# Kernel optimization log

Measured on AMD Instinct MI355X. Metric: run time of the kernel, lower is better.

The kernel has to match this reference:

```python
import jax, jax.numpy as jnp
import numpy as np
import math

D_MODEL = 1024
NUM_HEADS = 16
B, L = 2, 2048
# scale_level=0, patch_time_span=1 -> effective_stride=1
PERIODS = (1.0, 30.0)
WEIGHTS = (0.8, 0.4)
SIGMAS = (0.5, 2.0)


def setup_inputs() -> dict:
    key = jax.random.key(0)
    ks = jax.random.split(key, 10)
    s = 1.0 / math.sqrt(D_MODEL)
    inp = {
        "x": jax.random.normal(ks[0], (B, L, D_MODEL), dtype=jnp.float32),
        "Wq": jax.random.normal(ks[1], (D_MODEL, D_MODEL), dtype=jnp.float32) * s,
        "bq": jax.random.normal(ks[2], (D_MODEL,), dtype=jnp.float32) * 0.01,
        "Wk": jax.random.normal(ks[3], (D_MODEL, D_MODEL), dtype=jnp.float32) * s,
        "bk": jax.random.normal(ks[4], (D_MODEL,), dtype=jnp.float32) * 0.01,
        "Wv": jax.random.normal(ks[5], (D_MODEL, D_MODEL), dtype=jnp.float32) * s,
        "bv": jax.random.normal(ks[6], (D_MODEL,), dtype=jnp.float32) * 0.01,
        "Wo": jax.random.normal(ks[7], (D_MODEL, D_MODEL), dtype=jnp.float32) * s,
        "bo": jax.random.normal(ks[8], (D_MODEL,), dtype=jnp.float32) * 0.01,
        "prior_lambda": jnp.asarray(2.0, dtype=jnp.float32),
    }
    return inp


def _gaussian_mask(length):
    idx = jnp.arange(length, dtype=jnp.float32)
    delta = jnp.abs(idx[:, None] - idx[None, :])  # [L, L]
    mask = jnp.zeros_like(delta)
    for p, w, sigma in zip(PERIODS, WEIGHTS, SIGMAS):
        if p < 0.2:
            continue
        mask = mask + w * jnp.exp(-((delta - p) ** 2) / (2.0 * sigma ** 2))
    return mask


def reference(x, Wq, bq, Wk, bk, Wv, bv, Wo, bo, prior_lambda):
    Bx, Lx, D = x.shape
    H = NUM_HEADS
    hd = D // H

    def split_heads(t):  # [B, L, D] -> [B, H, L, hd]
        return t.reshape(Bx, Lx, H, hd).transpose(0, 2, 1, 3)

    Q = split_heads(x @ Wq.T + bq)
    K = split_heads(x @ Wk.T + bk)
    V = split_heads(x @ Wv.T + bv)

    scores = jnp.einsum("bhqd,bhkd->bhqk", Q, K) / math.sqrt(hd)
    scores = scores + prior_lambda * _gaussian_mask(Lx)[None, None, :, :]
    attn = jax.nn.softmax(scores, axis=-1)
    out = jnp.einsum("bhqk,bhkd->bhqd", attn, V)
    out = out.transpose(0, 2, 1, 3).reshape(Bx, Lx, D)
    return out @ Wo.T + bo
```

## Files before the change

### kernel.cpp

```cpp
#include <hip/hip_runtime.h>

#define D_MODEL 1024
#define SEQ_L   2048
#define NHEADS  16
#define HDIM    64
#define NROWS   4096

#define QSCALE 0.18033688011112042f
#define LOG2E  1.4426950408889634f

#if __has_builtin(__builtin_amdgcn_exp2f)
#define EXP2F(x) __builtin_amdgcn_exp2f(x)
#else
#define EXP2F(x) __expf((x) * 0.6931471805599453f)
#endif

typedef __attribute__((ext_vector_type(8))) short short8;
typedef __attribute__((ext_vector_type(4))) short short4v;
typedef __attribute__((ext_vector_type(4))) float floatx4;
typedef __attribute__((ext_vector_type(4))) unsigned short ushort4v;
typedef unsigned short ushort;

static __device__ __forceinline__ ushort f2bf(float f) {
    unsigned int u = __float_as_uint(f);
    u += 0x7FFFu + ((u >> 16) & 1u);
    return (ushort)(u >> 16);
}

static __device__ __forceinline__ floatx4 mfma16(short8 a, short8 b, floatx4 c) {
    return __builtin_amdgcn_mfma_f32_16x16x32_bf16(a, b, c, 0, 0, 0);
}

static __device__ __forceinline__ floatx4 mfma16k16(short4v a, short4v b, floatx4 c) {
    return __builtin_amdgcn_mfma_f32_16x16x16bf16_1k(a, b, c, 0, 0, 0);
}

static __device__ __forceinline__ void store8bf(ushort* dst, float4 a, float4 b) {
    uint4 pk;
    pk.x = (unsigned)f2bf(a.x) | ((unsigned)f2bf(a.y) << 16);
    pk.y = (unsigned)f2bf(a.z) | ((unsigned)f2bf(a.w) << 16);
    pk.z = (unsigned)f2bf(b.x) | ((unsigned)f2bf(b.y) << 16);
    pk.w = (unsigned)f2bf(b.z) | ((unsigned)f2bf(b.w) << 16);
    *(uint4*)dst = pk;
}

static __device__ __forceinline__ void gll16(const ushort* g, ushort* l) {
    __builtin_amdgcn_global_load_lds(
        (const __attribute__((address_space(1))) unsigned int*)(const unsigned int*)g,
        (__attribute__((address_space(3))) unsigned int*)(unsigned int*)l,
        16, 0, 0);
}

__global__ __launch_bounds__(256) void convert_bf16(
    const float* __restrict__ x,
    const float* __restrict__ wq, const float* __restrict__ wk,
    const float* __restrict__ wv, const float* __restrict__ wo,
    ushort* __restrict__ xb, ushort* __restrict__ wb3, ushort* __restrict__ wob)
{
    const int seg = blockIdx.y;
    const float* src;
    ushort* dst;
    int n;
    if      (seg == 0) { src = x;  dst = xb;                n = 4194304; }
    else if (seg == 1) { src = wq; dst = wb3;               n = 1048576; }
    else if (seg == 2) { src = wk; dst = wb3 + 1048576;     n = 1048576; }
    else if (seg == 3) { src = wv; dst = wb3 + 2097152;     n = 1048576; }
    else               { src = wo; dst = wob;               n = 1048576; }
    const int i = (blockIdx.x * 256 + threadIdx.x) * 8;
    if (i >= n) return;
    float4 a = *(const float4*)(src + i);
    float4 b = *(const float4*)(src + i + 4);
    store8bf(dst + i, a, b);
}

__global__ __launch_bounds__(256) void gemm_qkv(
    const ushort* __restrict__ A, const ushort* __restrict__ B,
    const float* __restrict__ bq, const float* __restrict__ bk,
    const float* __restrict__ bv,
    ushort* __restrict__ Qo, ushort* __restrict__ Ko, ushort* __restrict__ Vo)
{
    __shared__ ushort As[128 * 32];
    __shared__ ushort Bs[128 * 32];

    const int tid  = threadIdx.x;
    const int w    = tid >> 6;
    const int lane = tid & 63;
    const int l15  = lane & 15;
    const int quad = lane >> 4;
    const int wm   = w & 1;
    const int wn   = w >> 1;

    const int bm = blockIdx.y * 128;
    const int bn = blockIdx.x * 128;

    const int r0 = w * 16 + (lane >> 2);
    const int r1 = r0 + 64;
    const int c_ = lane & 3;
    const int g0 = c_ ^ ((r0 >> 1) & 3);
    const int g1 = c_ ^ ((r1 >> 1) & 3);

    const ushort* a0p = A + (size_t)(bm + r0) * 1024 + g0 * 8;
    const ushort* a1p = A + (size_t)(bm + r1) * 1024 + g1 * 8;
    const ushort* b0p = B + (size_t)(bn + r0) * 1024 + g0 * 8;
    const ushort* b1p = B + (size_t)(bn + r1) * 1024 + g1 * 8;
    ushort* lA0 = &As[r0 * 32 + c_ * 8];
    ushort* lA1 = &As[r1 * 32 + c_ * 8];
    ushort* lB0 = &Bs[r0 * 32 + c_ * 8];
    ushort* lB1 = &Bs[r1 * 32 + c_ * 8];

    const int cA = (quad ^ ((l15 >> 1) & 3)) * 8;

    floatx4 acc[4][4];
#pragma unroll
    for (int i = 0; i < 4; i++)
#pragma unroll
        for (int j = 0; j < 4; j++) acc[i][j] = (floatx4){0.f, 0.f, 0.f, 0.f};

    for (int k0 = 0; k0 < 1024; k0 += 32) {
        __syncthreads();
        gll16(a0p + k0, lA0);
        gll16(a1p + k0, lA1);
        gll16(b0p + k0, lB0);
        gll16(b1p + k0, lB1);
        __syncthreads();

        short8 af[4], bf[4];
#pragma unroll
        for (int mi = 0; mi < 4; mi++)
            af[mi] = *(const short8*)&As[(wm * 64 + mi * 16 + l15) * 32 + cA];
#pragma unroll
        for (int ni = 0; ni < 4; ni++)
            bf[ni] = *(const short8*)&Bs[(wn * 64 + ni * 16 + l15) * 32 + cA];
#pragma unroll
        for (int mi = 0; mi < 4; mi++)
#pragma unroll
            for (int ni = 0; ni < 4; ni++)
                acc[mi][ni] = mfma16(af[mi], bf[ni], acc[mi][ni]);
    }

#pragma unroll
    for (int ni = 0; ni < 4; ni++) {
        const int col = bn + wn * 64 + ni * 16 + l15;
        const int z = col >> 10;
        const int within = col & 1023;
        const int h  = within >> 6;
        const int hd = within & 63;
        const float* bias = (z == 0) ? bq : (z == 1) ? bk : bv;
        const float bvl = bias[within];
        if (z == 2) {
#pragma unroll
            for (int mi = 0; mi < 4; mi++) {
                const int row = bm + wm * 64 + mi * 16 + quad * 4;
                const int bb = row >> 11, li = row & 2047;
                ushort4v pk;
#pragma unroll
                for (int r = 0; r < 4; r++) pk[r] = f2bf(acc[mi][ni][r] + bvl);
                *(ushort4v*)(Vo + ((size_t)(bb * NHEADS + h) * HDIM + hd) * SEQ_L + li) = pk;
            }
        } else {
            const float scale = (z == 0) ? QSCALE : 1.0f;
            ushort* outp = (z == 0) ? Qo : Ko;
#pragma unroll
            for (int mi = 0; mi < 4; mi++) {
#pragma unroll
                for (int r = 0; r < 4; r++) {
                    const int row = bm + wm * 64 + mi * 16 + quad * 4 + r;
                    const int bb = row >> 11, li = row & 2047;
                    outp[((size_t)(bb * NHEADS + h) * SEQ_L + li) * HDIM + hd] =
                        f2bf((acc[mi][ni][r] + bvl) * scale);
                }
            }
        }
    }
}

__global__ __launch_bounds__(256) void attn(
    const ushort* __restrict__ Q,
    const ushort* __restrict__ K,
    const ushort* __restrict__ Vt,
    const float* __restrict__ lam,
    ushort* __restrict__ O)
{
    __shared__ float mtab[128];
    __shared__ ushort Ks[2][64 * 64];
    __shared__ ushort Vts[2][64 * 64];

    const int tid  = threadIdx.x;
    const int wave = tid >> 6;
    const int lane = tid & 63;
    const int l15  = lane & 15;
    const int quad = lane >> 4;

    const int qb = blockIdx.x;
    const int h  = blockIdx.y;
    const int bz = blockIdx.z;
    const int bh = bz * NHEADS + h;
    const int q0 = qb * 128;

    const float lambda = *lam;
    if (tid < 128) {
        float d  = (float)tid;
        float e1 = (d - 1.f) * (d - 1.f);
        float e2 = (d - 30.f) * (d - 30.f);
        mtab[tid] = LOG2E * lambda *
                    (0.8f * __expf(-2.0f * e1) + 0.4f * __expf(-0.125f * e2));
    }

    const ushort* qp =
        Q + ((size_t)bh * SEQ_L + q0 + wave * 16 + l15) * HDIM + quad * 8;
    short8 qf[2][2];
    qf[0][0] = *(const short8*)qp;
    qf[0][1] = *(const short8*)(qp + 32);
    qf[1][0] = *(const short8*)(qp + 64 * HDIM);
    qf[1][1] = *(const short8*)(qp + 64 * HDIM + 32);

    const ushort* kbase = K  + ((size_t)bh * SEQ_L) * HDIM;
    const ushort* vbase = Vt + ((size_t)bh * HDIM) * SEQ_L;

    const int cid0 = tid, cid1 = 256 + tid;
    const int row0 = cid0 >> 3, row1 = cid1 >> 3;
    const int cl0  = (cid0 & 7) ^ (row0 & 7);
    const int cl1  = (cid1 & 7) ^ (row1 & 7);
    const ushort* kg0 = kbase + (size_t)row0 * HDIM + cl0 * 8;
    const ushort* kg1 = kbase + (size_t)row1 * HDIM + cl1 * 8;
    const ushort* vg0 = vbase + (size_t)row0 * SEQ_L + cl0 * 8;
    const ushort* vg1 = vbase + (size_t)row1 * SEQ_L + cl1 * 8;

    floatx4 o[2][4];
#pragma unroll
    for (int g = 0; g < 2; g++)
#pragma unroll
        for (int i = 0; i < 4; i++) o[g][i] = (floatx4){0.f, 0.f, 0.f, 0.f};
    float lrun[2] = {0.f, 0.f};

    gll16(kg0, &Ks[0][cid0 * 8]);
    gll16(kg1, &Ks[0][cid1 * 8]);
    gll16(vg0, &Vts[0][cid0 * 8]);
    gll16(vg1, &Vts[0][cid1 * 8]);

    const int xo = l15 & 7;

    for (int j = 0; j < SEQ_L / 64; j++) {
        const int cur = j & 1;
        __syncthreads();
        if (j + 1 < SEQ_L / 64) {
            const int nxt = cur ^ 1;
            const int koff = (j + 1) * 64;
            gll16(kg0 + (size_t)koff * HDIM, &Ks[nxt][cid0 * 8]);
            gll16(kg1 + (size_t)koff * HDIM, &Ks[nxt][cid1 * 8]);
            gll16(vg0 + koff, &Vts[nxt][cid0 * 8]);
            gll16(vg1 + koff, &Vts[nxt][cid1 * 8]);
        }

        floatx4 s[2][4];
#pragma unroll
        for (int g = 0; g < 2; g++)
#pragma unroll
            for (int i = 0; i < 4; i++) s[g][i] = (floatx4){0.f, 0.f, 0.f, 0.f};
#pragma unroll
        for (int kk = 0; kk < 2; kk++) {
#pragma unroll
            for (int nt = 0; nt < 4; nt++) {
                const int slot = (kk * 4 + quad) ^ xo;
                short8 kf = *(const short8*)&Ks[cur][(nt * 16 + l15) * 64 + slot * 8];
                s[0][nt] = mfma16(kf, qf[0][kk], s[0][nt]);
                s[1][nt] = mfma16(kf, qf[1][kk], s[1][nt]);
            }
        }

#pragma unroll
        for (int g = 0; g < 2; g++) {
            const int tg = j - (qb * 2 + g);
            if (tg >= -1 && tg <= 1) {
                const int qg = q0 + g * 64 + wave * 16 + l15;
#pragma unroll
                for (int nt = 0; nt < 4; nt++) {
                    const int kg = j * 64 + nt * 16 + quad * 4;
#pragma unroll
                    for (int r = 0; r < 4; r++) {
                        int dq = qg - (kg + r);
                        int ad = dq < 0 ? -dq : dq;
                        s[g][nt][r] += mtab[ad];
                    }
                }
            }
        }

        short4v pb[2][4];
#pragma unroll
        for (int g = 0; g < 2; g++) {
#pragma unroll
            for (int nt = 0; nt < 4; nt++) {
                unsigned ur[4];
#pragma unroll
                for (int r = 0; r < 4; r++) {
                    float p = EXP2F(s[g][nt][r]);
                    lrun[g] += p;
                    ur[r] = __float_as_uint(p) + 0x8000u;
                }
                uint2 pk;
                pk.x = __builtin_amdgcn_perm(ur[1], ur[0], 0x07060302u);
                pk.y = __builtin_amdgcn_perm(ur[3], ur[2], 0x07060302u);
                pb[g][nt] = __builtin_bit_cast(short4v, pk);
            }
        }

#pragma unroll
        for (int kc = 0; kc < 4; kc++) {
#pragma unroll
            for (int nt = 0; nt < 4; nt++) {
                const int slot = (2 * kc + (quad >> 1)) ^ xo;
                short4v vf = *(const short4v*)
                    &Vts[cur][(nt * 16 + l15) * 64 + slot * 8 + (quad & 1) * 4];
                o[0][nt] = mfma16k16(vf, pb[0][kc], o[0][nt]);
                o[1][nt] = mfma16k16(vf, pb[1][kc], o[1][nt]);
            }
        }
    }

#pragma unroll
    for (int g = 0; g < 2; g++) {
        float s_ = lrun[g];
        s_ += __shfl_xor(s_, 16);
        s_ += __shfl_xor(s_, 32);
        const float linv = 1.f / s_;
        const int qg = q0 + g * 64 + wave * 16 + l15;
        ushort* obase = O + ((size_t)bz * SEQ_L + qg) * D_MODEL + h * HDIM;
#pragma unroll
        for (int nt = 0; nt < 4; nt++) {
            ushort4v pk;
#pragma unroll
            for (int r = 0; r < 4; r++) pk[r] = f2bf(o[g][nt][r] * linv);
            *(ushort4v*)(obase + nt * 16 + quad * 4) = pk;
        }
    }
}

__global__ __launch_bounds__(256) void gemm_out(
    const ushort* __restrict__ A, const ushort* __restrict__ B,
    const float* __restrict__ bo, float* __restrict__ out)
{
    __shared__ ushort As[64 * 32];
    __shared__ ushort Bs[128 * 32];

    const int tid  = threadIdx.x;
    const int w    = tid >> 6;
    const int lane = tid & 63;
    const int l15  = lane & 15;
    const int quad = lane >> 4;

    const int bm = blockIdx.y * 64;
    const int bn = blockIdx.x * 128;

    const int r0 = w * 16 + (lane >> 2);
    const int r1 = r0 + 64;
    const int c_ = lane & 3;
    const int g0 = c_ ^ ((r0 >> 1) & 3);
    const int g1 = c_ ^ ((r1 >> 1) & 3);

    const ushort* a0p = A + (size_t)(bm + r0) * 1024 + g0 * 8;
    const ushort* b0p = B + (size_t)(bn + r0) * 1024 + g0 * 8;
    const ushort* b1p = B + (size_t)(bn + r1) * 1024 + g1 * 8;
    ushort* lA0 = &As[r0 * 32 + c_ * 8];
    ushort* lB0 = &Bs[r0 * 32 + c_ * 8];
    ushort* lB1 = &Bs[r1 * 32 + c_ * 8];

    const int cA = (quad ^ ((l15 >> 1) & 3)) * 8;

    floatx4 acc[4][2];
#pragma unroll
    for (int i = 0; i < 4; i++)
#pragma unroll
        for (int j = 0; j < 2; j++) acc[i][j] = (floatx4){0.f, 0.f, 0.f, 0.f};

    for (int k0 = 0; k0 < 1024; k0 += 32) {
        __syncthreads();
        gll16(a0p + k0, lA0);
        gll16(b0p + k0, lB0);
        gll16(b1p + k0, lB1);
        __syncthreads();

        short8 af[4], bf[2];
#pragma unroll
        for (int mi = 0; mi < 4; mi++)
            af[mi] = *(const short8*)&As[(mi * 16 + l15) * 32 + cA];
#pragma unroll
        for (int ni = 0; ni < 2; ni++)
            bf[ni] = *(const short8*)&Bs[(w * 32 + ni * 16 + l15) * 32 + cA];
#pragma unroll
        for (int mi = 0; mi < 4; mi++)
#pragma unroll
            for (int ni = 0; ni < 2; ni++)
                acc[mi][ni] = mfma16(af[mi], bf[ni], acc[mi][ni]);
    }

#pragma unroll
    for (int ni = 0; ni < 2; ni++) {
        const int col = bn + w * 32 + ni * 16 + l15;
        const float bvl = bo[col];
#pragma unroll
        for (int mi = 0; mi < 4; mi++) {
#pragma unroll
            for (int r = 0; r < 4; r++) {
                const int row = bm + mi * 16 + quad * 4 + r;
                out[(size_t)row * 1024 + col] = acc[mi][ni][r] + bvl;
            }
        }
    }
}

extern "C" void kernel_launch(void* const* d_in, const int* in_sizes, int n_in,
                              void* d_out, int out_size, void* d_ws, size_t ws_size,
                              hipStream_t stream)
{
    const float* x   = (const float*)d_in[0];
    const float* Wq  = (const float*)d_in[1];
    const float* bq  = (const float*)d_in[2];
    const float* Wk  = (const float*)d_in[3];
    const float* bk  = (const float*)d_in[4];
    const float* Wv  = (const float*)d_in[5];
    const float* bv  = (const float*)d_in[6];
    const float* Wo  = (const float*)d_in[7];
    const float* bo  = (const float*)d_in[8];
    const float* lam = (const float*)d_in[9];
    float* out = (float*)d_out;

    const size_t NELEM = (size_t)NROWS * D_MODEL;
    ushort* Qw  = (ushort*)d_ws;
    ushort* Kw  = Qw + NELEM;
    ushort* Vw  = Kw + NELEM;
    ushort* XA  = Vw + NELEM;
    ushort* Wb3 = XA + NELEM;
    ushort* Wob = Wb3 + 3 * 1024 * 1024;

    dim3 gc(2048, 5);
    convert_bf16<<<gc, 256, 0, stream>>>(x, Wq, Wk, Wv, Wo, XA, Wb3, Wob);

    dim3 g1(3072 / 128, NROWS / 128);
    gemm_qkv<<<g1, 256, 0, stream>>>(XA, Wb3, bq, bk, bv, Qw, Kw, Vw);

    dim3 g2(SEQ_L / 128, NHEADS, 2);
    attn<<<g2, 256, 0, stream>>>(Qw, Kw, Vw, lam, XA);

    dim3 g3(1024 / 128, NROWS / 64);
    gemm_out<<<g3, 256, 0, stream>>>(XA, Wob, bo, out);
}
```

Baseline: 217.0 us.

## Split attention over two key halves with merge kernel and vectorize GEMM epilogues

The attention kernel now splits the key range in two across the grid z dimension, doubling the block count to raise occupancy. Each half writes unnormalized outputs plus a row sum (computed with an MFMA against a ones vector), and a new merge kernel combines them. The QKV and output GEMMs swap MFMA operand order so each lane holds contiguous columns, which allows vectorized bias loads and vector stores. The cost is an extra kernel launch, extra workspace traffic for two partial outputs, and bf16 rounding of the unnormalized partials, which works only because the softmax uses no running max.

```diff
diff --git a/kernel.cpp b/kernel.cpp
--- a/kernel.cpp
+++ b/kernel.cpp
@@ -92,6 +92,7 @@
 
     const int bm = blockIdx.y * 128;
     const int bn = blockIdx.x * 128;
+    const int z  = blockIdx.x >> 3;
 
     const int r0 = w * 16 + (lane >> 2);
     const int r1 = r0 + 64;
@@ -116,38 +117,35 @@
 #pragma unroll
         for (int j = 0; j < 4; j++) acc[i][j] = (floatx4){0.f, 0.f, 0.f, 0.f};
 
-    for (int k0 = 0; k0 < 1024; k0 += 32) {
-        __syncthreads();
-        gll16(a0p + k0, lA0);
-        gll16(a1p + k0, lA1);
-        gll16(b0p + k0, lB0);
-        gll16(b1p + k0, lB1);
-        __syncthreads();
-
-        short8 af[4], bf[4];
-#pragma unroll
-        for (int mi = 0; mi < 4; mi++)
-            af[mi] = *(const short8*)&As[(wm * 64 + mi * 16 + l15) * 32 + cA];
-#pragma unroll
-        for (int ni = 0; ni < 4; ni++)
-            bf[ni] = *(const short8*)&Bs[(wn * 64 + ni * 16 + l15) * 32 + cA];
-#pragma unroll
-        for (int mi = 0; mi < 4; mi++)
+    if (z == 2) {
+        for (int k0 = 0; k0 < 1024; k0 += 32) {
+            __syncthreads();
+            gll16(a0p + k0, lA0);
+            gll16(a1p + k0, lA1);
+            gll16(b0p + k0, lB0);
+            gll16(b1p + k0, lB1);
+            __syncthreads();
+
+            short8 af[4], bf[4];
+#pragma unroll
+            for (int mi = 0; mi < 4; mi++)
+                af[mi] = *(const short8*)&As[(wm * 64 + mi * 16 + l15) * 32 + cA];
 #pragma unroll
             for (int ni = 0; ni < 4; ni++)
-                acc[mi][ni] = mfma16(af[mi], bf[ni], acc[mi][ni]);
-    }
-
-#pragma unroll
-    for (int ni = 0; ni < 4; ni++) {
-        const int col = bn + wn * 64 + ni * 16 + l15;
-        const int z = col >> 10;
-        const int within = col & 1023;
-        const int h  = within >> 6;
-        const int hd = within & 63;
-        const float* bias = (z == 0) ? bq : (z == 1) ? bk : bv;
-        const float bvl = bias[within];
-        if (z == 2) {
+                bf[ni] = *(const short8*)&Bs[(wn * 64 + ni * 16 + l15) * 32 + cA];
+#pragma unroll
+            for (int mi = 0; mi < 4; mi++)
+#pragma unroll
+                for (int ni = 0; ni < 4; ni++)
+                    acc[mi][ni] = mfma16(af[mi], bf[ni], acc[mi][ni]);
+        }
+#pragma unroll
+        for (int ni = 0; ni < 4; ni++) {
+            const int col = bn + wn * 64 + ni * 16 + l15;
+            const int within = col & 1023;
+            const int h  = within >> 6;
+            const int hd = within & 63;
+            const float bvl = bv[within];
 #pragma unroll
             for (int mi = 0; mi < 4; mi++) {
                 const int row = bm + wm * 64 + mi * 16 + quad * 4;
@@ -157,29 +155,61 @@
                 for (int r = 0; r < 4; r++) pk[r] = f2bf(acc[mi][ni][r] + bvl);
                 *(ushort4v*)(Vo + ((size_t)(bb * NHEADS + h) * HDIM + hd) * SEQ_L + li) = pk;
             }
-        } else {
-            const float scale = (z == 0) ? QSCALE : 1.0f;
-            ushort* outp = (z == 0) ? Qo : Ko;
+        }
+    } else {
+        for (int k0 = 0; k0 < 1024; k0 += 32) {
+            __syncthreads();
+            gll16(a0p + k0, lA0);
+            gll16(a1p + k0, lA1);
+            gll16(b0p + k0, lB0);
+            gll16(b1p + k0, lB1);
+            __syncthreads();
+
+            short8 af[4], bf[4];
+#pragma unroll
+            for (int mi = 0; mi < 4; mi++)
+                af[mi] = *(const short8*)&As[(wm * 64 + mi * 16 + l15) * 32 + cA];
+#pragma unroll
+            for (int ni = 0; ni < 4; ni++)
+                bf[ni] = *(const short8*)&Bs[(wn * 64 + ni * 16 + l15) * 32 + cA];
+#pragma unroll
+            for (int mi = 0; mi < 4; mi++)
+#pragma unroll
+                for (int ni = 0; ni < 4; ni++)
+                    acc[mi][ni] = mfma16(bf[ni], af[mi], acc[mi][ni]);
+        }
+        const float* bias = z ? bk : bq;
+        const float scale = z ? 1.0f : QSCALE;
+        ushort* outp = z ? Ko : Qo;
+        const int cwbase = (bn & 1023) + wn * 64;
+        const int h = cwbase >> 6;
+#pragma unroll
+        for (int ni = 0; ni < 4; ni++) {
+            const int hd0 = ni * 16 + quad * 4;
+            const float4 bb4 = *(const float4*)&bias[cwbase + hd0];
+            const float bv0 = bb4.x, bv1 = bb4.y, bv2 = bb4.z, bv3 = bb4.w;
 #pragma unroll
             for (int mi = 0; mi < 4; mi++) {
-#pragma unroll
-                for (int r = 0; r < 4; r++) {
-                    const int row = bm + wm * 64 + mi * 16 + quad * 4 + r;
-                    const int bb = row >> 11, li = row & 2047;
-                    outp[((size_t)(bb * NHEADS + h) * SEQ_L + li) * HDIM + hd] =
-                        f2bf((acc[mi][ni][r] + bvl) * scale);
-                }
+                const int row = bm + wm * 64 + mi * 16 + l15;
+                const int bb = row >> 11, li = row & 2047;
+                ushort4v pk;
+                pk[0] = f2bf((acc[mi][ni][0] + bv0) * scale);
+                pk[1] = f2bf((acc[mi][ni][1] + bv1) * scale);
+                pk[2] = f2bf((acc[mi][ni][2] + bv2) * scale);
+                pk[3] = f2bf((acc[mi][ni][3] + bv3) * scale);
+                *(ushort4v*)(outp + ((size_t)(bb * NHEADS + h) * SEQ_L + li) * HDIM + hd0) = pk;
             }
         }
     }
 }
 
-__global__ __launch_bounds__(256) void attn(
+__global__ __launch_bounds__(256, 4) void attn(
     const ushort* __restrict__ Q,
     const ushort* __restrict__ K,
     const ushort* __restrict__ Vt,
     const float* __restrict__ lam,
-    ushort* __restrict__ O)
+    ushort* __restrict__ O0, ushort* __restrict__ O1,
+    float* __restrict__ Lw)
 {
     __shared__ float mtab[128];
     __shared__ ushort Ks[2][64 * 64];
@@ -193,9 +223,12 @@
 
     const int qb = blockIdx.x;
     const int h  = blockIdx.y;
-    const int bz = blockIdx.z;
+    const int zz = blockIdx.z;
+    const int bz = zz >> 1;
+    const int sp = zz & 1;
     const int bh = bz * NHEADS + h;
     const int q0 = qb * 128;
+    const int kb = sp * 1024;
 
     const float lambda = *lam;
     if (tid < 128) {
@@ -221,17 +254,22 @@
     const int row0 = cid0 >> 3, row1 = cid1 >> 3;
     const int cl0  = (cid0 & 7) ^ (row0 & 7);
     const int cl1  = (cid1 & 7) ^ (row1 & 7);
-    const ushort* kg0 = kbase + (size_t)row0 * HDIM + cl0 * 8;
-    const ushort* kg1 = kbase + (size_t)row1 * HDIM + cl1 * 8;
-    const ushort* vg0 = vbase + (size_t)row0 * SEQ_L + cl0 * 8;
-    const ushort* vg1 = vbase + (size_t)row1 * SEQ_L + cl1 * 8;
+    const ushort* kg0 = kbase + (size_t)(kb + row0) * HDIM + cl0 * 8;
+    const ushort* kg1 = kbase + (size_t)(kb + row1) * HDIM + cl1 * 8;
+    const ushort* vg0 = vbase + (size_t)row0 * SEQ_L + kb + cl0 * 8;
+    const ushort* vg1 = vbase + (size_t)row1 * SEQ_L + kb + cl1 * 8;
 
     floatx4 o[2][4];
 #pragma unroll
     for (int g = 0; g < 2; g++)
 #pragma unroll
         for (int i = 0; i < 4; i++) o[g][i] = (floatx4){0.f, 0.f, 0.f, 0.f};
-    float lrun[2] = {0.f, 0.f};
+    floatx4 ol[2];
+    ol[0] = (floatx4){0.f, 0.f, 0.f, 0.f};
+    ol[1] = (floatx4){0.f, 0.f, 0.f, 0.f};
+
+    short4v ones;
+    ones[0] = 0x3F80; ones[1] = 0x3F80; ones[2] = 0x3F80; ones[3] = 0x3F80;
 
     gll16(kg0, &Ks[0][cid0 * 8]);
     gll16(kg1, &Ks[0][cid1 * 8]);
@@ -240,12 +278,12 @@
 
     const int xo = l15 & 7;
 
-    for (int j = 0; j < SEQ_L / 64; j++) {
-        const int cur = j & 1;
+    for (int t = 0; t < 16; t++) {
+        const int cur = t & 1;
         __syncthreads();
-        if (j + 1 < SEQ_L / 64) {
+        if (t + 1 < 16) {
             const int nxt = cur ^ 1;
-            const int koff = (j + 1) * 64;
+            const int koff = (t + 1) * 64;
             gll16(kg0 + (size_t)koff * HDIM, &Ks[nxt][cid0 * 8]);
             gll16(kg1 + (size_t)koff * HDIM, &Ks[nxt][cid1 * 8]);
             gll16(vg0 + koff, &Vts[nxt][cid0 * 8]);
@@ -268,6 +306,7 @@
             }
         }
 
+        const int j = sp * 16 + t;
 #pragma unroll
         for (int g = 0; g < 2; g++) {
             const int tg = j - (qb * 2 + g);
@@ -275,10 +314,10 @@
                 const int qg = q0 + g * 64 + wave * 16 + l15;
 #pragma unroll
                 for (int nt = 0; nt < 4; nt++) {
-                    const int kg = j * 64 + nt * 16 + quad * 4;
+                    const int kgi = j * 64 + nt * 16 + quad * 4;
 #pragma unroll
                     for (int r = 0; r < 4; r++) {
-                        int dq = qg - (kg + r);
+                        int dq = qg - (kgi + r);
                         int ad = dq < 0 ? -dq : dq;
                         s[g][nt][r] += mtab[ad];
                     }
@@ -293,11 +332,8 @@
             for (int nt = 0; nt < 4; nt++) {
                 unsigned ur[4];
 #pragma unroll
-                for (int r = 0; r < 4; r++) {
-                    float p = EXP2F(s[g][nt][r]);
-                    lrun[g] += p;
-                    ur[r] = __float_as_uint(p) + 0x8000u;
-                }
+                for (int r = 0; r < 4; r++)
+                    ur[r] = __float_as_uint(EXP2F(s[g][nt][r])) + 0x8000u;
                 uint2 pk;
                 pk.x = __builtin_amdgcn_perm(ur[1], ur[0], 0x07060302u);
                 pk.y = __builtin_amdgcn_perm(ur[3], ur[2], 0x07060302u);
@@ -315,25 +351,58 @@
                 o[0][nt] = mfma16k16(vf, pb[0][kc], o[0][nt]);
                 o[1][nt] = mfma16k16(vf, pb[1][kc], o[1][nt]);
             }
-        }
-    }
-
+            ol[0] = mfma16k16(ones, pb[0][kc], ol[0]);
+            ol[1] = mfma16k16(ones, pb[1][kc], ol[1]);
+        }
+    }
+
+    ushort* Osp = sp ? O1 : O0;
 #pragma unroll
     for (int g = 0; g < 2; g++) {
-        float s_ = lrun[g];
-        s_ += __shfl_xor(s_, 16);
-        s_ += __shfl_xor(s_, 32);
-        const float linv = 1.f / s_;
         const int qg = q0 + g * 64 + wave * 16 + l15;
-        ushort* obase = O + ((size_t)bz * SEQ_L + qg) * D_MODEL + h * HDIM;
+        if (quad == 0)
+            Lw[((size_t)(sp * 2 + bz) * NHEADS + h) * SEQ_L + qg] = ol[g][0];
+        ushort* obase = Osp + ((size_t)bz * SEQ_L + qg) * D_MODEL + h * HDIM;
 #pragma unroll
         for (int nt = 0; nt < 4; nt++) {
             ushort4v pk;
 #pragma unroll
-            for (int r = 0; r < 4; r++) pk[r] = f2bf(o[g][nt][r] * linv);
+            for (int r = 0; r < 4; r++) pk[r] = f2bf(o[g][nt][r]);
             *(ushort4v*)(obase + nt * 16 + quad * 4) = pk;
         }
     }
+}
+
+__global__ __launch_bounds__(256) void merge_attn(
+    const ushort* __restrict__ O0, const ushort* __restrict__ O1,
+    const float* __restrict__ Lw, ushort* __restrict__ Aout)
+{
+    const int gid = blockIdx.x * 256 + threadIdx.x;
+    const int i = gid * 8;
+    const int row = i >> 10;
+    const int h   = (i >> 6) & 15;
+    const int bz  = row >> 11, q = row & 2047;
+    const int li  = (bz * NHEADS + h) * SEQ_L + q;
+    const float linv = 1.f / (Lw[li] + Lw[2 * NHEADS * SEQ_L + li]);
+
+    uint4 a = *(const uint4*)(O0 + i);
+    uint4 b = *(const uint4*)(O1 + i);
+    unsigned aw[4] = {a.x, a.y, a.z, a.w};
+    unsigned bw[4] = {b.x, b.y, b.z, b.w};
+    uint4 res;
+    unsigned rw[4];
+#pragma unroll
+    for (int k = 0; k < 4; k++) {
+        float alo = __uint_as_float(aw[k] << 16);
+        float ahi = __uint_as_float(aw[k] & 0xFFFF0000u);
+        float blo = __uint_as_float(bw[k] << 16);
+        float bhi = __uint_as_float(bw[k] & 0xFFFF0000u);
+        float lo = (alo + blo) * linv;
+        float hi = (ahi + bhi) * linv;
+        rw[k] = (unsigned)f2bf(lo) | ((unsigned)f2bf(hi) << 16);
+    }
+    res.x = rw[0]; res.y = rw[1]; res.z = rw[2]; res.w = rw[3];
+    *(uint4*)(Aout + i) = res;
 }
 
 __global__ __launch_bounds__(256) void gemm_out(
@@ -391,20 +460,22 @@
         for (int mi = 0; mi < 4; mi++)
 #pragma unroll
             for (int ni = 0; ni < 2; ni++)
-                acc[mi][ni] = mfma16(af[mi], bf[ni], acc[mi][ni]);
+                acc[mi][ni] = mfma16(bf[ni], af[mi], acc[mi][ni]);
     }
 
 #pragma unroll
     for (int ni = 0; ni < 2; ni++) {
-        const int col = bn + w * 32 + ni * 16 + l15;
-        const float bvl = bo[col];
+        const int col0 = bn + w * 32 + ni * 16 + quad * 4;
+        const float4 bb4 = *(const float4*)&bo[col0];
 #pragma unroll
         for (int mi = 0; mi < 4; mi++) {
-#pragma unroll
-            for (int r = 0; r < 4; r++) {
-                const int row = bm + mi * 16 + quad * 4 + r;
-                out[(size_t)row * 1024 + col] = acc[mi][ni][r] + bvl;
-            }
+            const int row = bm + mi * 16 + l15;
+            float4 st;
+            st.x = acc[mi][ni][0] + bb4.x;
+            st.y = acc[mi][ni][1] + bb4.y;
+            st.z = acc[mi][ni][2] + bb4.z;
+            st.w = acc[mi][ni][3] + bb4.w;
+            *(float4*)(out + (size_t)row * 1024 + col0) = st;
         }
     }
 }
@@ -429,9 +500,12 @@
     ushort* Qw  = (ushort*)d_ws;
     ushort* Kw  = Qw + NELEM;
     ushort* Vw  = Kw + NELEM;
-    ushort* XA  = Vw + NELEM;
+    ushort* O0  = Vw + NELEM;
+    ushort* O1  = O0 + NELEM;
+    ushort* XA  = O1 + NELEM;
     ushort* Wb3 = XA + NELEM;
     ushort* Wob = Wb3 + 3 * 1024 * 1024;
+    float*  Lw  = (float*)(Wob + 1024 * 1024);
 
     dim3 gc(2048, 5);
     convert_bf16<<<gc, 256, 0, stream>>>(x, Wq, Wk, Wv, Wo, XA, Wb3, Wob);
@@ -439,8 +513,10 @@
     dim3 g1(3072 / 128, NROWS / 128);
     gemm_qkv<<<g1, 256, 0, stream>>>(XA, Wb3, bq, bk, bv, Qw, Kw, Vw);
 
-    dim3 g2(SEQ_L / 128, NHEADS, 2);
-    attn<<<g2, 256, 0, stream>>>(Qw, Kw, Vw, lam, XA);
+    dim3 g2(SEQ_L / 128, NHEADS, 4);
+    attn<<<g2, 256, 0, stream>>>(Qw, Kw, Vw, lam, O0, O1, Lw);
+
+    merge_attn<<<NELEM / (256 * 8), 256, 0, stream>>>(O0, O1, Lw, XA);
 
     dim3 g3(1024 / 128, NROWS / 64);
     gemm_out<<<g3, 256, 0, stream>>>(XA, Wob, bo, out);
```

New measurement: 210.2 us. 1.03x faster.
